# Optimization experiments

Measured on AMD Instinct MI355X. Metric: run time of the kernel, lower is better.

The kernel has to match this reference:

```python
import jax, jax.numpy as jnp
import numpy as np

MASK_VALUE = -1e6  # torch code uses -1000000.0, not -inf


def setup_inputs() -> dict:
    key = jax.random.key(0)
    k1, k2, k3, k4 = jax.random.split(key, 4)
    B, Nq, Nk, d = 32, 2048, 2048, 128
    return {
        "querys": jax.random.normal(k1, (B, Nq, d), dtype=jnp.float32),
        "keys": jax.random.normal(k2, (B, Nk, d), dtype=jnp.float32),
        "values": jax.random.normal(k3, (B, Nk, d), dtype=jnp.float32),
        "valid_seq_len": jax.random.randint(k4, (B,), 1, Nk + 1, dtype=jnp.int32),
    }


def reference(querys, keys, values, valid_seq_len):
    # querys: [B, Nq, d], keys/values: [B, Nk, d], valid_seq_len: [B]
    d = querys.shape[-1]
    scale = 1.0 / jnp.sqrt(jnp.asarray(d, dtype=querys.dtype))
    # scores: [B, Nq, Nk]
    scores = jnp.einsum("bqd,bkd->bqk", querys, keys) * scale
    Nk = keys.shape[1]
    # mask key positions >= valid length (per batch, broadcast over queries)
    mask = jnp.arange(Nk, dtype=jnp.int32)[None, None, :] < valid_seq_len[:, None, None]
    scores = jnp.where(mask, scores, jnp.asarray(MASK_VALUE, dtype=scores.dtype))
    attn = jax.nn.softmax(scores, axis=-1)
    # dropout prob = 0.0 -> identity
    out = jnp.einsum("bqk,bkd->bqd", attn, values)
    return out
```

## Files before the change

### kernel.cpp

```cpp
#include <hip/hip_runtime.h>
#include <cstdint>
#include <math.h>

typedef unsigned short ushort_t;
typedef unsigned int uint_t;
typedef __bf16 v8bf __attribute__((ext_vector_type(8)));
typedef float v16f __attribute__((ext_vector_type(16)));

constexpr int B_SZ = 32, NQ = 2048, NK = 2048, DH = 128;
constexpr int BQ2 = 128, BK = 64;
constexpr int NQT = NQ / BQ2;
constexpr float SCALE = 0.08838834764831845f;
constexpr float M_FIX = 12.0f;

__device__ inline int swzK(int row, int chunk) {
  return row * 128 + ((chunk ^ (row & 7)) << 3);
}
__device__ inline int swzV(int d, int chunk) {
  return d * 64 + ((chunk ^ (d & 7)) << 3);
}

__device__ inline v8bf cvt8(const float* __restrict__ p) {
  float4 f0 = *reinterpret_cast<const float4*>(p);
  float4 f1 = *reinterpret_cast<const float4*>(p + 4);
  v8bf r;
  r[0] = (__bf16)f0.x; r[1] = (__bf16)f0.y; r[2] = (__bf16)f0.z; r[3] = (__bf16)f0.w;
  r[4] = (__bf16)f1.x; r[5] = (__bf16)f1.y; r[6] = (__bf16)f1.z; r[7] = (__bf16)f1.w;
  return r;
}

__device__ inline v8bf cvt8s(const float* __restrict__ p, float s) {
  float4 f0 = *reinterpret_cast<const float4*>(p);
  float4 f1 = *reinterpret_cast<const float4*>(p + 4);
  v8bf r;
  r[0] = (__bf16)(f0.x * s); r[1] = (__bf16)(f0.y * s);
  r[2] = (__bf16)(f0.z * s); r[3] = (__bf16)(f0.w * s);
  r[4] = (__bf16)(f1.x * s); r[5] = (__bf16)(f1.y * s);
  r[6] = (__bf16)(f1.z * s); r[7] = (__bf16)(f1.w * s);
  return r;
}

__device__ inline v8bf cvt8r(const float4 f0, const float4 f1) {
  v8bf r;
  r[0] = (__bf16)f0.x; r[1] = (__bf16)f0.y; r[2] = (__bf16)f0.z; r[3] = (__bf16)f0.w;
  r[4] = (__bf16)f1.x; r[5] = (__bf16)f1.y; r[6] = (__bf16)f1.z; r[7] = (__bf16)f1.w;
  return r;
}

__device__ inline uint_t pk2(float a, float b) {
  const ushort_t ua = __builtin_bit_cast(ushort_t, (__bf16)a);
  const ushort_t ub = __builtin_bit_cast(ushort_t, (__bf16)b);
  return (uint_t)ua | ((uint_t)ub << 16);
}

__global__ __launch_bounds__(256) void transpose_v(const float* __restrict__ V,
                                                   ushort_t* __restrict__ Vt) {
  __shared__ __align__(16) ushort_t st[64 * 128];
  const int b = blockIdx.y, k0 = blockIdx.x * 64, t = threadIdx.x;
  for (int c = 0; c < 4; ++c) {
    const int row = (t >> 4) + 16 * c;
    const int col = (t & 15) * 8;
    v8bf v = cvt8(V + ((size_t)(b * NK + k0 + row)) * DH + col);
    const int chunk = (col >> 3) ^ ((row >> 3) & 7);
    *reinterpret_cast<v8bf*>(&st[row * 128 + chunk * 8]) = v;
  }
  __syncthreads();
  for (int c = 0; c < 4; ++c) {
    const int d = (t >> 3) + 32 * c;
    const int kc = (t & 7) * 8;
    alignas(16) ushort_t tmp[8];
    for (int j = 0; j < 8; ++j) {
      const int row = kc + j;
      const int elem = (d & 7) | (((d >> 3) ^ ((row >> 3) & 7)) << 3);
      tmp[j] = st[row * 128 + elem];
    }
    *reinterpret_cast<uint4*>(Vt + ((size_t)(b * DH + d)) * NK + k0 + kc) =
        *reinterpret_cast<const uint4*>(tmp);
  }
}

__global__ __launch_bounds__(256, 2) void attn(const float* __restrict__ Q,
                                               const float* __restrict__ K,
                                               const ushort_t* __restrict__ Vt,
                                               const int* __restrict__ vsl,
                                               float* __restrict__ Out) {
  __shared__ __align__(16) ushort_t sK2[2][64 * 128];
  __shared__ __align__(16) ushort_t sV2[2][DH * 64];

  const int t = threadIdx.x;
  const int lane = t & 63, w = t >> 6, hi = lane >> 5, l32 = lane & 31;

  int* s_ord = reinterpret_cast<int*>(sK2);
  if (t < 32) {
    const int cx = (vsl[t] + 63) >> 6;
    int rank = 0;
    for (int y = 0; y < 32; ++y) {
      const int cy = (vsl[y] + 63) >> 6;
      rank += (cy > cx) || (cy == cx && y < t);
    }
    s_ord[rank] = t;
  }
  __syncthreads();
  const int n = (int)blockIdx.x;
  const int ci = n & 255, cj = n >> 8;
  const int ru = cj ? 511 - ci : ci;
  const int b = s_ord[ru >> 4];
  const int qt2 = ru & 15;
  __syncthreads();

  const int q0 = qt2 * BQ2;
  const int valid = vsl[b];
  const int nt = (valid + BK - 1) / BK;

  v8bf qf[8];
  {
    const float* qp = Q + ((size_t)(b * NQ + q0 + w * 32 + l32)) * DH + hi * 8;
#pragma unroll
    for (int ks = 0; ks < 8; ++ks) qf[ks] = cvt8s(qp + ks * 16, SCALE);
  }

  v16f o[4];
#pragma unroll
  for (int nb = 0; nb < 4; ++nb)
#pragma unroll
    for (int r = 0; r < 16; ++r) o[nb][r] = 0.f;
  float lsum = 0.f;

  const float* Kb = K + (size_t)b * NK * DH;
  const ushort_t* Vb = Vt + (size_t)b * DH * NK;
  const int krow = t >> 4, kch = t & 15;
  const int vd = t >> 3, vch = t & 7;

  float4 k0a, k0b, k1a, k1b, k2a, k2b, k3a, k3b;
  uint4 v0r, v1r, v2r, v3r;

#define LD4F(p) (*reinterpret_cast<const float4*>(p))
#define LD4U(p) (*reinterpret_cast<const uint4*>(p))
#define PREFETCH(KOFF)                                                   \
  do {                                                                   \
    const float* p0_ = Kb + (size_t)((KOFF) + krow) * DH + kch * 8;      \
    const float* p1_ = Kb + (size_t)((KOFF) + krow + 16) * DH + kch * 8; \
    const float* p2_ = Kb + (size_t)((KOFF) + krow + 32) * DH + kch * 8; \
    const float* p3_ = Kb + (size_t)((KOFF) + krow + 48) * DH + kch * 8; \
    k0a = LD4F(p0_); k0b = LD4F(p0_ + 4);                                \
    k1a = LD4F(p1_); k1b = LD4F(p1_ + 4);                                \
    k2a = LD4F(p2_); k2b = LD4F(p2_ + 4);                                \
    k3a = LD4F(p3_); k3b = LD4F(p3_ + 4);                                \
    const ushort_t* q0_ = Vb + (size_t)(vd)*NK + (KOFF) + vch * 8;       \
    const ushort_t* q1_ = Vb + (size_t)(vd + 32) * NK + (KOFF) + vch * 8;\
    const ushort_t* q2_ = Vb + (size_t)(vd + 64) * NK + (KOFF) + vch * 8;\
    const ushort_t* q3_ = Vb + (size_t)(vd + 96) * NK + (KOFF) + vch * 8;\
    v0r = LD4U(q0_); v1r = LD4U(q1_); v2r = LD4U(q2_); v3r = LD4U(q3_);  \
  } while (0)

  PREFETCH(0);
  int cur = 0;
  for (int tile = 0; tile < nt; ++tile) {
    const int k0 = tile * BK;
    ushort_t* sk = sK2[cur];
    ushort_t* sv = sV2[cur];
    *reinterpret_cast<v8bf*>(&sk[swzK(krow + 0, kch)]) = cvt8r(k0a, k0b);
    *reinterpret_cast<v8bf*>(&sk[swzK(krow + 16, kch)]) = cvt8r(k1a, k1b);
    *reinterpret_cast<v8bf*>(&sk[swzK(krow + 32, kch)]) = cvt8r(k2a, k2b);
    *reinterpret_cast<v8bf*>(&sk[swzK(krow + 48, kch)]) = cvt8r(k3a, k3b);
    *reinterpret_cast<uint4*>(&sv[swzV(vd + 0, vch)]) = v0r;
    *reinterpret_cast<uint4*>(&sv[swzV(vd + 32, vch)]) = v1r;
    *reinterpret_cast<uint4*>(&sv[swzV(vd + 64, vch)]) = v2r;
    *reinterpret_cast<uint4*>(&sv[swzV(vd + 96, vch)]) = v3r;
    if (tile + 1 < nt) PREFETCH(k0 + BK);
    __syncthreads();

    const bool part = (k0 + BK > valid);
    const int rowA = l32;

#pragma unroll
    for (int kb = 0; kb < 2; ++kb) {
      const uint4 kf0 = LD4U(&sk[swzK(kb * 32 + rowA, 0 + hi)]);
      const uint4 kf1 = LD4U(&sk[swzK(kb * 32 + rowA, 2 + hi)]);
      const uint4 kf2 = LD4U(&sk[swzK(kb * 32 + rowA, 4 + hi)]);
      const uint4 kf3 = LD4U(&sk[swzK(kb * 32 + rowA, 6 + hi)]);
      const uint4 kf4 = LD4U(&sk[swzK(kb * 32 + rowA, 8 + hi)]);
      const uint4 kf5 = LD4U(&sk[swzK(kb * 32 + rowA, 10 + hi)]);
      const uint4 kf6 = LD4U(&sk[swzK(kb * 32 + rowA, 12 + hi)]);
      const uint4 kf7 = LD4U(&sk[swzK(kb * 32 + rowA, 14 + hi)]);
      v16f sa;
#pragma unroll
      for (int r = 0; r < 16; ++r) sa[r] = 0.f;
      __builtin_amdgcn_s_setprio(1);
      sa = __builtin_amdgcn_mfma_f32_32x32x16_bf16(__builtin_bit_cast(v8bf, kf0), qf[0], sa, 0, 0, 0);
      sa = __builtin_amdgcn_mfma_f32_32x32x16_bf16(__builtin_bit_cast(v8bf, kf1), qf[1], sa, 0, 0, 0);
      sa = __builtin_amdgcn_mfma_f32_32x32x16_bf16(__builtin_bit_cast(v8bf, kf2), qf[2], sa, 0, 0, 0);
      sa = __builtin_amdgcn_mfma_f32_32x32x16_bf16(__builtin_bit_cast(v8bf, kf3), qf[3], sa, 0, 0, 0);
      sa = __builtin_amdgcn_mfma_f32_32x32x16_bf16(__builtin_bit_cast(v8bf, kf4), qf[4], sa, 0, 0, 0);
      sa = __builtin_amdgcn_mfma_f32_32x32x16_bf16(__builtin_bit_cast(v8bf, kf5), qf[5], sa, 0, 0, 0);
      sa = __builtin_amdgcn_mfma_f32_32x32x16_bf16(__builtin_bit_cast(v8bf, kf6), qf[6], sa, 0, 0, 0);
      sa = __builtin_amdgcn_mfma_f32_32x32x16_bf16(__builtin_bit_cast(v8bf, kf7), qf[7], sa, 0, 0, 0);
      __builtin_amdgcn_s_setprio(0);
      float p[16];
#pragma unroll
      for (int r = 0; r < 16; ++r) {
        const int crow = (r & 3) + 8 * (r >> 2) + 4 * hi;
        float x = sa[r];
        if (part) x = (k0 + kb * 32 + crow < valid) ? x : -1e30f;
        const float e = __expf(x - M_FIX);
        p[r] = e;
        lsum += e;
      }
#pragma unroll
      for (int q2 = 0; q2 < 2; ++q2) {
        const int ksg = 2 * kb + q2;
        const uint4 vf0 = LD4U(&sv[swzV(0 + l32, 2 * ksg + hi)]);
        const uint4 vf1 = LD4U(&sv[swzV(32 + l32, 2 * ksg + hi)]);
        const uint4 vf2 = LD4U(&sv[swzV(64 + l32, 2 * ksg + hi)]);
        const uint4 vf3 = LD4U(&sv[swzV(96 + l32, 2 * ksg + hi)]);
        uint_t A0 = pk2(p[8 * q2 + 0], p[8 * q2 + 1]);
        uint_t A1 = pk2(p[8 * q2 + 2], p[8 * q2 + 3]);
        uint_t B0 = pk2(p[8 * q2 + 4], p[8 * q2 + 5]);
        uint_t B1 = pk2(p[8 * q2 + 6], p[8 * q2 + 7]);
        asm("v_permlane32_swap_b32 %0, %1" : "+v"(A0), "+v"(B0));
        asm("v_permlane32_swap_b32 %0, %1" : "+v"(A1), "+v"(B1));
        uint4 fw;
        fw.x = A0; fw.y = A1; fw.z = B0; fw.w = B1;
        const v8bf pa = __builtin_bit_cast(v8bf, fw);
        __builtin_amdgcn_s_setprio(1);
        o[0] = __builtin_amdgcn_mfma_f32_32x32x16_bf16(pa, __builtin_bit_cast(v8bf, vf0), o[0], 0, 0, 0);
        o[1] = __builtin_amdgcn_mfma_f32_32x32x16_bf16(pa, __builtin_bit_cast(v8bf, vf1), o[1], 0, 0, 0);
        o[2] = __builtin_amdgcn_mfma_f32_32x32x16_bf16(pa, __builtin_bit_cast(v8bf, vf2), o[2], 0, 0, 0);
        o[3] = __builtin_amdgcn_mfma_f32_32x32x16_bf16(pa, __builtin_bit_cast(v8bf, vf3), o[3], 0, 0, 0);
        __builtin_amdgcn_s_setprio(0);
      }
    }
    cur ^= 1;
  }

  const float rs = lsum + __shfl_xor(lsum, 32);
  const float inv_own = 1.0f / rs;
#pragma unroll
  for (int r = 0; r < 16; ++r) {
    const int crow = (r & 3) + 8 * (r >> 2) + 4 * hi;
    const float inv = __shfl(inv_own, crow);
    float* op = Out + ((size_t)(b * NQ + q0 + w * 32 + crow)) * DH + l32;
#pragma unroll
    for (int nb = 0; nb < 4; ++nb) op[nb * 32] = o[nb][r] * inv;
  }
#undef PREFETCH
#undef LD4F
#undef LD4U
}

extern "C" void kernel_launch(void* const* d_in, const int* in_sizes, int n_in,
                              void* d_out, int out_size, void* d_ws, size_t ws_size,
                              hipStream_t stream) {
  const float* Q = (const float*)d_in[0];
  const float* K = (const float*)d_in[1];
  const float* V = (const float*)d_in[2];
  const int* vsl = (const int*)d_in[3];
  float* Out = (float*)d_out;
  ushort_t* Vt = (ushort_t*)d_ws;

  transpose_v<<<dim3(NK / 64, B_SZ), dim3(256), 0, stream>>>(V, Vt);
  attn<<<dim3(B_SZ * NQT), dim3(256), 0, stream>>>(Q, K, Vt, vsl, Out);
}
```

Before: 191.9 us.

## Software-pipeline QK softmax of next tile with PV of current tile; use exp2

Restructures the main loop so the QK^T MFMAs and exponentials for tile t+1 are issued in the same iteration as the PV MFMAs for tile t, with staging and prefetch shifted one tile ahead and a second barrier per iteration. Q is pre-scaled by log2(e)/sqrt(d) and the fixed max offset is converted to base 2, so the exponential becomes a raw v_exp_f32 instead of __expf. The row-sum accumulator is split into two partial sums to shorten the dependency chain. The aim is to overlap softmax ALU work with matrix-core work, at the cost of extra live registers and one more barrier per tile, which may reduce occupancy.

Result: slower. 198.2 us (+3.3%).

```diff
diff --git a/kernel.cpp b/kernel.cpp
--- a/kernel.cpp
+++ b/kernel.cpp
@@ -10,8 +10,8 @@
 constexpr int B_SZ = 32, NQ = 2048, NK = 2048, DH = 128;
 constexpr int BQ2 = 128, BK = 64;
 constexpr int NQT = NQ / BQ2;
-constexpr float SCALE = 0.08838834764831845f;
-constexpr float M_FIX = 12.0f;
+constexpr float QSCALE = 0.12751880226116815f;
+constexpr float M2 = 17.312340490667561f;
 
 __device__ inline int swzK(int row, int chunk) {
   return row * 128 + ((chunk ^ (row & 7)) << 3);
@@ -20,9 +20,16 @@
   return d * 64 + ((chunk ^ (d & 7)) << 3);
 }
 
+__device__ __forceinline__ float4 ld4f(const float* p) {
+  return *reinterpret_cast<const float4*>(p);
+}
+__device__ __forceinline__ uint4 ld4u(const ushort_t* p) {
+  return *reinterpret_cast<const uint4*>(p);
+}
+
 __device__ inline v8bf cvt8(const float* __restrict__ p) {
-  float4 f0 = *reinterpret_cast<const float4*>(p);
-  float4 f1 = *reinterpret_cast<const float4*>(p + 4);
+  float4 f0 = ld4f(p);
+  float4 f1 = ld4f(p + 4);
   v8bf r;
   r[0] = (__bf16)f0.x; r[1] = (__bf16)f0.y; r[2] = (__bf16)f0.z; r[3] = (__bf16)f0.w;
   r[4] = (__bf16)f1.x; r[5] = (__bf16)f1.y; r[6] = (__bf16)f1.z; r[7] = (__bf16)f1.w;
@@ -30,8 +37,8 @@
 }
 
 __device__ inline v8bf cvt8s(const float* __restrict__ p, float s) {
-  float4 f0 = *reinterpret_cast<const float4*>(p);
-  float4 f1 = *reinterpret_cast<const float4*>(p + 4);
+  float4 f0 = ld4f(p);
+  float4 f1 = ld4f(p + 4);
   v8bf r;
   r[0] = (__bf16)(f0.x * s); r[1] = (__bf16)(f0.y * s);
   r[2] = (__bf16)(f0.z * s); r[3] = (__bf16)(f0.w * s);
@@ -47,7 +54,7 @@
   return r;
 }
 
-__device__ inline uint_t pk2(float a, float b) {
+__device__ __forceinline__ uint_t pk2(float a, float b) {
   const ushort_t ua = __builtin_bit_cast(ushort_t, (__bf16)a);
   const ushort_t ub = __builtin_bit_cast(ushort_t, (__bf16)b);
   return (uint_t)ua | ((uint_t)ub << 16);
@@ -79,6 +86,77 @@
   }
 }
 
+__device__ __forceinline__ void qk_sm(const ushort_t* sk, int l32, int hi, int k0n,
+                                      int valid, const v8bf* qf, float& ls0,
+                                      float& ls1, uint4& pa0, uint4& pa1,
+                                      uint4& pa2, uint4& pa3) {
+  const bool part = (k0n + BK > valid);
+#pragma unroll
+  for (int kb = 0; kb < 2; ++kb) {
+    const int rowA = kb * 32 + l32;
+    const uint4 kf0 = ld4u(&sk[swzK(rowA, 0 + hi)]);
+    const uint4 kf1 = ld4u(&sk[swzK(rowA, 2 + hi)]);
+    const uint4 kf2 = ld4u(&sk[swzK(rowA, 4 + hi)]);
+    const uint4 kf3 = ld4u(&sk[swzK(rowA, 6 + hi)]);
+    const uint4 kf4 = ld4u(&sk[swzK(rowA, 8 + hi)]);
+    const uint4 kf5 = ld4u(&sk[swzK(rowA, 10 + hi)]);
+    const uint4 kf6 = ld4u(&sk[swzK(rowA, 12 + hi)]);
+    const uint4 kf7 = ld4u(&sk[swzK(rowA, 14 + hi)]);
+    v16f sa;
+#pragma unroll
+    for (int r = 0; r < 16; ++r) sa[r] = 0.f;
+    __builtin_amdgcn_s_setprio(1);
+    sa = __builtin_amdgcn_mfma_f32_32x32x16_bf16(__builtin_bit_cast(v8bf, kf0), qf[0], sa, 0, 0, 0);
+    sa = __builtin_amdgcn_mfma_f32_32x32x16_bf16(__builtin_bit_cast(v8bf, kf1), qf[1], sa, 0, 0, 0);
+    sa = __builtin_amdgcn_mfma_f32_32x32x16_bf16(__builtin_bit_cast(v8bf, kf2), qf[2], sa, 0, 0, 0);
+    sa = __builtin_amdgcn_mfma_f32_32x32x16_bf16(__builtin_bit_cast(v8bf, kf3), qf[3], sa, 0, 0, 0);
+    sa = __builtin_amdgcn_mfma_f32_32x32x16_bf16(__builtin_bit_cast(v8bf, kf4), qf[4], sa, 0, 0, 0);
+    sa = __builtin_amdgcn_mfma_f32_32x32x16_bf16(__builtin_bit_cast(v8bf, kf5), qf[5], sa, 0, 0, 0);
+    sa = __builtin_amdgcn_mfma_f32_32x32x16_bf16(__builtin_bit_cast(v8bf, kf6), qf[6], sa, 0, 0, 0);
+    sa = __builtin_amdgcn_mfma_f32_32x32x16_bf16(__builtin_bit_cast(v8bf, kf7), qf[7], sa, 0, 0, 0);
+    __builtin_amdgcn_s_setprio(0);
+    float p[16];
+#pragma unroll
+    for (int r = 0; r < 16; ++r) {
+      const int crow = (r & 3) + 8 * (r >> 2) + 4 * hi;
+      float x = sa[r];
+      if (part) x = (k0n + kb * 32 + crow < valid) ? x : -1e30f;
+      float e;
+      asm("v_exp_f32 %0, %1" : "=v"(e) : "v"(x - M2));
+      p[r] = e;
+      if (r < 8) ls0 += e; else ls1 += e;
+    }
+#pragma unroll
+    for (int q2 = 0; q2 < 2; ++q2) {
+      uint_t A0 = pk2(p[8 * q2 + 0], p[8 * q2 + 1]);
+      uint_t A1 = pk2(p[8 * q2 + 2], p[8 * q2 + 3]);
+      uint_t B0 = pk2(p[8 * q2 + 4], p[8 * q2 + 5]);
+      uint_t B1 = pk2(p[8 * q2 + 6], p[8 * q2 + 7]);
+      asm("v_permlane32_swap_b32 %0, %1" : "+v"(A0), "+v"(B0));
+      asm("v_permlane32_swap_b32 %0, %1" : "+v"(A1), "+v"(B1));
+      uint4 fw;
+      fw.x = A0; fw.y = A1; fw.z = B0; fw.w = B1;
+      if (kb == 0) { if (q2 == 0) pa0 = fw; else pa1 = fw; }
+      else         { if (q2 == 0) pa2 = fw; else pa3 = fw; }
+    }
+  }
+}
+
+__device__ __forceinline__ void pv4(const ushort_t* sv, int l32, int hi,
+                                    const uint4 paf, int ksg, v16f* o) {
+  const uint4 vf0 = ld4u(&sv[swzV(0 + l32, 2 * ksg + hi)]);
+  const uint4 vf1 = ld4u(&sv[swzV(32 + l32, 2 * ksg + hi)]);
+  const uint4 vf2 = ld4u(&sv[swzV(64 + l32, 2 * ksg + hi)]);
+  const uint4 vf3 = ld4u(&sv[swzV(96 + l32, 2 * ksg + hi)]);
+  const v8bf pa = __builtin_bit_cast(v8bf, paf);
+  __builtin_amdgcn_s_setprio(1);
+  o[0] = __builtin_amdgcn_mfma_f32_32x32x16_bf16(pa, __builtin_bit_cast(v8bf, vf0), o[0], 0, 0, 0);
+  o[1] = __builtin_amdgcn_mfma_f32_32x32x16_bf16(pa, __builtin_bit_cast(v8bf, vf1), o[1], 0, 0, 0);
+  o[2] = __builtin_amdgcn_mfma_f32_32x32x16_bf16(pa, __builtin_bit_cast(v8bf, vf2), o[2], 0, 0, 0);
+  o[3] = __builtin_amdgcn_mfma_f32_32x32x16_bf16(pa, __builtin_bit_cast(v8bf, vf3), o[3], 0, 0, 0);
+  __builtin_amdgcn_s_setprio(0);
+}
+
 __global__ __launch_bounds__(256, 2) void attn(const float* __restrict__ Q,
                                                const float* __restrict__ K,
                                                const ushort_t* __restrict__ Vt,
@@ -116,7 +194,7 @@
   {
     const float* qp = Q + ((size_t)(b * NQ + q0 + w * 32 + l32)) * DH + hi * 8;
 #pragma unroll
-    for (int ks = 0; ks < 8; ++ks) qf[ks] = cvt8s(qp + ks * 16, SCALE);
+    for (int ks = 0; ks < 8; ++ks) qf[ks] = cvt8s(qp + ks * 16, QSCALE);
   }
 
   v16f o[4];
@@ -124,7 +202,7 @@
   for (int nb = 0; nb < 4; ++nb)
 #pragma unroll
     for (int r = 0; r < 16; ++r) o[nb][r] = 0.f;
-  float lsum = 0.f;
+  float ls0 = 0.f, ls1 = 0.f;
 
   const float* Kb = K + (size_t)b * NK * DH;
   const ushort_t* Vb = Vt + (size_t)b * DH * NK;
@@ -134,105 +212,60 @@
   float4 k0a, k0b, k1a, k1b, k2a, k2b, k3a, k3b;
   uint4 v0r, v1r, v2r, v3r;
 
-#define LD4F(p) (*reinterpret_cast<const float4*>(p))
-#define LD4U(p) (*reinterpret_cast<const uint4*>(p))
 #define PREFETCH(KOFF)                                                   \
   do {                                                                   \
     const float* p0_ = Kb + (size_t)((KOFF) + krow) * DH + kch * 8;      \
     const float* p1_ = Kb + (size_t)((KOFF) + krow + 16) * DH + kch * 8; \
     const float* p2_ = Kb + (size_t)((KOFF) + krow + 32) * DH + kch * 8; \
     const float* p3_ = Kb + (size_t)((KOFF) + krow + 48) * DH + kch * 8; \
-    k0a = LD4F(p0_); k0b = LD4F(p0_ + 4);                                \
-    k1a = LD4F(p1_); k1b = LD4F(p1_ + 4);                                \
-    k2a = LD4F(p2_); k2b = LD4F(p2_ + 4);                                \
-    k3a = LD4F(p3_); k3b = LD4F(p3_ + 4);                                \
+    k0a = ld4f(p0_); k0b = ld4f(p0_ + 4);                                \
+    k1a = ld4f(p1_); k1b = ld4f(p1_ + 4);                                \
+    k2a = ld4f(p2_); k2b = ld4f(p2_ + 4);                                \
+    k3a = ld4f(p3_); k3b = ld4f(p3_ + 4);                                \
     const ushort_t* q0_ = Vb + (size_t)(vd)*NK + (KOFF) + vch * 8;       \
     const ushort_t* q1_ = Vb + (size_t)(vd + 32) * NK + (KOFF) + vch * 8;\
     const ushort_t* q2_ = Vb + (size_t)(vd + 64) * NK + (KOFF) + vch * 8;\
     const ushort_t* q3_ = Vb + (size_t)(vd + 96) * NK + (KOFF) + vch * 8;\
-    v0r = LD4U(q0_); v1r = LD4U(q1_); v2r = LD4U(q2_); v3r = LD4U(q3_);  \
+    v0r = ld4u(q0_); v1r = ld4u(q1_); v2r = ld4u(q2_); v3r = ld4u(q3_);  \
   } while (0)
 
+#define STAGE(SK_, SV_)                                                      \
+  do {                                                                       \
+    *reinterpret_cast<v8bf*>(&(SK_)[swzK(krow + 0, kch)]) = cvt8r(k0a, k0b); \
+    *reinterpret_cast<v8bf*>(&(SK_)[swzK(krow + 16, kch)]) = cvt8r(k1a, k1b);\
+    *reinterpret_cast<v8bf*>(&(SK_)[swzK(krow + 32, kch)]) = cvt8r(k2a, k2b);\
+    *reinterpret_cast<v8bf*>(&(SK_)[swzK(krow + 48, kch)]) = cvt8r(k3a, k3b);\
+    *reinterpret_cast<uint4*>(&(SV_)[swzV(vd + 0, vch)]) = v0r;              \
+    *reinterpret_cast<uint4*>(&(SV_)[swzV(vd + 32, vch)]) = v1r;             \
+    *reinterpret_cast<uint4*>(&(SV_)[swzV(vd + 64, vch)]) = v2r;             \
+    *reinterpret_cast<uint4*>(&(SV_)[swzV(vd + 96, vch)]) = v3r;             \
+  } while (0)
+
   PREFETCH(0);
-  int cur = 0;
+  STAGE(sK2[0], sV2[0]);
+  if (nt > 1) PREFETCH(BK);
+  __syncthreads();
+  uint4 pa0, pa1, pa2, pa3;
+  qk_sm(sK2[0], l32, hi, 0, valid, qf, ls0, ls1, pa0, pa1, pa2, pa3);
+
   for (int tile = 0; tile < nt; ++tile) {
-    const int k0 = tile * BK;
-    ushort_t* sk = sK2[cur];
-    ushort_t* sv = sV2[cur];
-    *reinterpret_cast<v8bf*>(&sk[swzK(krow + 0, kch)]) = cvt8r(k0a, k0b);
-    *reinterpret_cast<v8bf*>(&sk[swzK(krow + 16, kch)]) = cvt8r(k1a, k1b);
-    *reinterpret_cast<v8bf*>(&sk[swzK(krow + 32, kch)]) = cvt8r(k2a, k2b);
-    *reinterpret_cast<v8bf*>(&sk[swzK(krow + 48, kch)]) = cvt8r(k3a, k3b);
-    *reinterpret_cast<uint4*>(&sv[swzV(vd + 0, vch)]) = v0r;
-    *reinterpret_cast<uint4*>(&sv[swzV(vd + 32, vch)]) = v1r;
-    *reinterpret_cast<uint4*>(&sv[swzV(vd + 64, vch)]) = v2r;
-    *reinterpret_cast<uint4*>(&sv[swzV(vd + 96, vch)]) = v3r;
-    if (tile + 1 < nt) PREFETCH(k0 + BK);
+    const int cur = tile & 1;
+    if (tile + 1 < nt) {
+      STAGE(sK2[cur ^ 1], sV2[cur ^ 1]);
+      if (tile + 2 < nt) PREFETCH((tile + 2) * BK);
+    }
     __syncthreads();
-
-    const bool part = (k0 + BK > valid);
-    const int rowA = l32;
-
-#pragma unroll
-    for (int kb = 0; kb < 2; ++kb) {
-      const uint4 kf0 = LD4U(&sk[swzK(kb * 32 + rowA, 0 + hi)]);
-      const uint4 kf1 = LD4U(&sk[swzK(kb * 32 + rowA, 2 + hi)]);
-      const uint4 kf2 = LD4U(&sk[swzK(kb * 32 + rowA, 4 + hi)]);
-      const uint4 kf3 = LD4U(&sk[swzK(kb * 32 + rowA, 6 + hi)]);
-      const uint4 kf4 = LD4U(&sk[swzK(kb * 32 + rowA, 8 + hi)]);
-      const uint4 kf5 = LD4U(&sk[swzK(kb * 32 + rowA, 10 + hi)]);
-      const uint4 kf6 = LD4U(&sk[swzK(kb * 32 + rowA, 12 + hi)]);
-      const uint4 kf7 = LD4U(&sk[swzK(kb * 32 + rowA, 14 + hi)]);
-      v16f sa;
-#pragma unroll
-      for (int r = 0; r < 16; ++r) sa[r] = 0.f;
-      __builtin_amdgcn_s_setprio(1);
-      sa = __builtin_amdgcn_mfma_f32_32x32x16_bf16(__builtin_bit_cast(v8bf, kf0), qf[0], sa, 0, 0, 0);
-      sa = __builtin_amdgcn_mfma_f32_32x32x16_bf16(__builtin_bit_cast(v8bf, kf1), qf[1], sa, 0, 0, 0);
-      sa = __builtin_amdgcn_mfma_f32_32x32x16_bf16(__builtin_bit_cast(v8bf, kf2), qf[2], sa, 0, 0, 0);
-      sa = __builtin_amdgcn_mfma_f32_32x32x16_bf16(__builtin_bit_cast(v8bf, kf3), qf[3], sa, 0, 0, 0);
-      sa = __builtin_amdgcn_mfma_f32_32x32x16_bf16(__builtin_bit_cast(v8bf, kf4), qf[4], sa, 0, 0, 0);
-      sa = __builtin_amdgcn_mfma_f32_32x32x16_bf16(__builtin_bit_cast(v8bf, kf5), qf[5], sa, 0, 0, 0);
-      sa = __builtin_amdgcn_mfma_f32_32x32x16_bf16(__builtin_bit_cast(v8bf, kf6), qf[6], sa, 0, 0, 0);
-      sa = __builtin_amdgcn_mfma_f32_32x32x16_bf16(__builtin_bit_cast(v8bf, kf7), qf[7], sa, 0, 0, 0);
-      __builtin_amdgcn_s_setprio(0);
-      float p[16];
-#pragma unroll
-      for (int r = 0; r < 16; ++r) {
-        const int crow = (r & 3) + 8 * (r >> 2) + 4 * hi;
-        float x = sa[r];
-        if (part) x = (k0 + kb * 32 + crow < valid) ? x : -1e30f;
-        const float e = __expf(x - M_FIX);
-        p[r] = e;
-        lsum += e;
-      }
-#pragma unroll
-      for (int q2 = 0; q2 < 2; ++q2) {
-        const int ksg = 2 * kb + q2;
-        const uint4 vf0 = LD4U(&sv[swzV(0 + l32, 2 * ksg + hi)]);
-        const uint4 vf1 = LD4U(&sv[swzV(32 + l32, 2 * ksg + hi)]);
-        const uint4 vf2 = LD4U(&sv[swzV(64 + l32, 2 * ksg + hi)]);
-        const uint4 vf3 = LD4U(&sv[swzV(96 + l32, 2 * ksg + hi)]);
-        uint_t A0 = pk2(p[8 * q2 + 0], p[8 * q2 + 1]);
-        uint_t A1 = pk2(p[8 * q2 + 2], p[8 * q2 + 3]);
-        uint_t B0 = pk2(p[8 * q2 + 4], p[8 * q2 + 5]);
-        uint_t B1 = pk2(p[8 * q2 + 6], p[8 * q2 + 7]);
-        asm("v_permlane32_swap_b32 %0, %1" : "+v"(A0), "+v"(B0));
-        asm("v_permlane32_swap_b32 %0, %1" : "+v"(A1), "+v"(B1));
-        uint4 fw;
-        fw.x = A0; fw.y = A1; fw.z = B0; fw.w = B1;
-        const v8bf pa = __builtin_bit_cast(v8bf, fw);
-        __builtin_amdgcn_s_setprio(1);
-        o[0] = __builtin_amdgcn_mfma_f32_32x32x16_bf16(pa, __builtin_bit_cast(v8bf, vf0), o[0], 0, 0, 0);
-        o[1] = __builtin_amdgcn_mfma_f32_32x32x16_bf16(pa, __builtin_bit_cast(v8bf, vf1), o[1], 0, 0, 0);
-        o[2] = __builtin_amdgcn_mfma_f32_32x32x16_bf16(pa, __builtin_bit_cast(v8bf, vf2), o[2], 0, 0, 0);
-        o[3] = __builtin_amdgcn_mfma_f32_32x32x16_bf16(pa, __builtin_bit_cast(v8bf, vf3), o[3], 0, 0, 0);
-        __builtin_amdgcn_s_setprio(0);
-      }
-    }
-    cur ^= 1;
-  }
-
+    pv4(sV2[cur], l32, hi, pa0, 0, o);
+    pv4(sV2[cur], l32, hi, pa1, 1, o);
+    pv4(sV2[cur], l32, hi, pa2, 2, o);
+    pv4(sV2[cur], l32, hi, pa3, 3, o);
+    if (tile + 1 < nt)
+      qk_sm(sK2[cur ^ 1], l32, hi, (tile + 1) * BK, valid, qf, ls0, ls1, pa0, pa1,
+            pa2, pa3);
+    __syncthreads();
+  }
+
+  const float lsum = ls0 + ls1;
   const float rs = lsum + __shfl_xor(lsum, 32);
   const float inv_own = 1.0f / rs;
 #pragma unroll
@@ -244,8 +277,7 @@
     for (int nb = 0; nb < 4; ++nb) op[nb * 32] = o[nb][r] * inv;
   }
 #undef PREFETCH
-#undef LD4F
-#undef LD4U
+#undef STAGE
 }
 
 extern "C" void kernel_launch(void* const* d_in, const int* in_sizes, int n_in,
```
